# Performance work log

Measured on AMD Instinct MI355X. Metric: run time of the kernel, lower is better.

## Reference

```python
import jax, jax.numpy as jnp
import numpy as np

N0 = 50000
N1 = 50000
E = 500000
IN_DIM = 128
OUT_DIM = 128
H = 8
DK = OUT_DIM // H  # 16
SQRT_DK = float(np.sqrt(DK))
NUM_TYPES = 2
NUM_REL = 3
# relations: (src_type, dst_type, e_id)
RELATIONS = [(0, 1, 0), (1, 0, 1), (0, 0, 2)]


def setup_inputs() -> dict:
    key = jax.random.key(0)
    ks = jax.random.split(key, 24)
    d = {}
    d["h0"] = jax.random.normal(ks[0], (N0, IN_DIM), dtype=jnp.float32)
    d["h1"] = jax.random.normal(ks[1], (N1, IN_DIM), dtype=jnp.float32)
    d["src0"] = jax.random.randint(ks[2], (E,), 0, N0)
    d["dst0"] = jax.random.randint(ks[3], (E,), 0, N1)
    d["src1"] = jax.random.randint(ks[4], (E,), 0, N1)
    d["dst1"] = jax.random.randint(ks[5], (E,), 0, N0)
    d["src2"] = jax.random.randint(ks[6], (E,), 0, N0)
    d["dst2"] = jax.random.randint(ks[7], (E,), 0, N0)
    w_scale = 1.0 / np.sqrt(IN_DIM)
    # per-node-type stacked linear weights (k, q, v, a), torch Linear convention: y = x @ W.T + b
    d["Wk"] = jax.random.normal(ks[8], (NUM_TYPES, OUT_DIM, IN_DIM), dtype=jnp.float32) * w_scale
    d["bk"] = jnp.zeros((NUM_TYPES, OUT_DIM), dtype=jnp.float32)
    d["Wq"] = jax.random.normal(ks[9], (NUM_TYPES, OUT_DIM, IN_DIM), dtype=jnp.float32) * w_scale
    d["bq"] = jnp.zeros((NUM_TYPES, OUT_DIM), dtype=jnp.float32)
    d["Wv"] = jax.random.normal(ks[10], (NUM_TYPES, OUT_DIM, IN_DIM), dtype=jnp.float32) * w_scale
    d["bv"] = jnp.zeros((NUM_TYPES, OUT_DIM), dtype=jnp.float32)
    d["Wa"] = jax.random.normal(ks[11], (NUM_TYPES, OUT_DIM, OUT_DIM), dtype=jnp.float32) * w_scale
    d["ba"] = jnp.zeros((NUM_TYPES, OUT_DIM), dtype=jnp.float32)
    xavier = float(np.sqrt(6.0 / (DK + DK)))
    d["rel_att"] = jax.random.uniform(ks[12], (NUM_REL, H, DK, DK), dtype=jnp.float32, minval=-xavier, maxval=xavier)
    d["rel_msg"] = jax.random.uniform(ks[13], (NUM_REL, H, DK, DK), dtype=jnp.float32, minval=-xavier, maxval=xavier)
    d["rel_pri"] = jnp.ones((NUM_REL, H), dtype=jnp.float32)
    d["skip"] = jnp.ones((NUM_TYPES,), dtype=jnp.float32)
    return d


def _lin(x, W, b):
    return x @ W.T + b


def reference(h0, h1, src0, dst0, src1, dst1, src2, dst2,
              Wk, bk, Wq, bq, Wv, bv, Wa, ba,
              rel_att, rel_msg, rel_pri, skip):
    h = [h0, h1]
    edges = [(src0, dst0), (src1, dst1), (src2, dst2)]
    # per-type projections, reshaped to (N, H, DK)
    k = [_lin(h[t], Wk[t], bk[t]).reshape(-1, H, DK) for t in range(NUM_TYPES)]
    q = [_lin(h[t], Wq[t], bq[t]).reshape(-1, H, DK) for t in range(NUM_TYPES)]
    v = [_lin(h[t], Wv[t], bv[t]).reshape(-1, H, DK) for t in range(NUM_TYPES)]

    agg = [[] for _ in range(NUM_TYPES)]
    for (s, dt, e), (src, dst) in zip(RELATIONS, edges):
        # relation-specific transforms of source k and v
        kr = jnp.einsum('nhi,hij->nhj', k[s], rel_att[e])
        vr = jnp.einsum('nhi,hij->nhj', v[s], rel_msg[e])
        # per-edge dot-product score (E, H)
        score = (q[dt][dst] * kr[src]).sum(-1) * rel_pri[e] / SQRT_DK
        n_dst = h[dt].shape[0]
        # edge softmax normalized by dst (stable)
        m = jax.ops.segment_max(score, dst, num_segments=n_dst)
        ex = jnp.exp(score - m[dst])
        den = jax.ops.segment_sum(ex, dst, num_segments=n_dst)
        attn = ex / den[dst]  # (E, H)
        # weighted message scatter-sum -> (n_dst, H, DK)
        msg = vr[src] * attn[:, :, None]
        agg[dt].append(jax.ops.segment_sum(msg, dst, num_segments=n_dst))

    new_h = []
    for t in range(NUM_TYPES):
        # cross_reducer='mean' over relations targeting this node type
        tmean = sum(agg[t]) / float(len(agg[t]))
        tflat = tmean.reshape(-1, OUT_DIM)
        trans = _lin(tflat, Wa[t], ba[t])  # dropout = identity (eval)
        alpha = jax.nn.sigmoid(skip[t])
        new_h.append(trans * alpha + h[t] * (1.0 - alpha))
    return tuple(new_h)
```

## Files before the change

kernel.cpp:

```cpp
#include <hip/hip_runtime.h>

typedef __attribute__((ext_vector_type(8))) _Float16 half8;
typedef __attribute__((ext_vector_type(2))) _Float16 half2v;
typedef __attribute__((ext_vector_type(4))) float f32x4;

#define NB 196
#define CHK 2048
#define CAPB 4096
#define PSTRIDE 6144

__device__ __forceinline__ unsigned short f2h(float f) {
  _Float16 h = (_Float16)f;
  return __builtin_bit_cast(unsigned short, h);
}
__device__ __forceinline__ float fdot2(unsigned a, unsigned b, float c) {
  return __builtin_amdgcn_fdot2(__builtin_bit_cast(half2v, a), __builtin_bit_cast(half2v, b), c,
                                false);
}

#define DPPADD(v, ctrl) \
  ((v) + __int_as_float(__builtin_amdgcn_update_dpp(0, __float_as_int(v), ctrl, 0xF, 0xF, true)))

__global__ void cvt2_kernel(const float* __restrict__ a, unsigned short* __restrict__ oa,
                            const float* __restrict__ b, unsigned short* __restrict__ ob,
                            int n8) {
  int i = blockIdx.x * 256 + threadIdx.x;
  if (i >= n8) return;
  const float* in = blockIdx.y ? b : a;
  unsigned short* out = blockIdx.y ? ob : oa;
  const float4* p = (const float4*)(in + (size_t)i * 8);
  float4 x = p[0], y = p[1];
  uint4 v;
  v.x = f2h(x.x) | ((unsigned)f2h(x.y) << 16);
  v.y = f2h(x.z) | ((unsigned)f2h(x.w) << 16);
  v.z = f2h(y.x) | ((unsigned)f2h(y.y) << 16);
  v.w = f2h(y.z) | ((unsigned)f2h(y.w) << 16);
  *(uint4*)(out + (size_t)i * 8) = v;
}

__global__ void compose_w_kernel(const float* __restrict__ Wk, const float* __restrict__ bk,
                                 const float* __restrict__ Wv, const float* __restrict__ bv,
                                 const float* __restrict__ rel_att, const float* __restrict__ rel_msg,
                                 const float* __restrict__ rel_pri,
                                 unsigned short* __restrict__ Wkr, float* __restrict__ bkr,
                                 unsigned short* __restrict__ Wvr, float* __restrict__ bvr) {
  int e = blockIdx.x;
  int o = blockIdx.y;
  int z = blockIdx.z;
  int c = threadIdx.x;
  int hd = o >> 4, j = o & 15;
  const int se[3] = {0, 1, 0};
  int s = se[e];
  const float* W = z ? Wv : Wk;
  const float* b = z ? bv : bk;
  const float* R = z ? rel_msg : rel_att;
  float scale = z ? 1.0f : (rel_pri[e * 8 + hd] * 0.25f);
  float acc = 0.0f, bacc = 0.0f;
#pragma unroll
  for (int i = 0; i < 16; ++i) {
    float r = R[((e * 8 + hd) * 16 + i) * 16 + j];
    acc += W[(s * 128 + hd * 16 + i) * 128 + c] * r;
    bacc += b[s * 128 + hd * 16 + i] * r;
  }
  unsigned short* Wo = z ? Wvr : Wkr;
  float* bo = z ? bvr : bkr;
  Wo[((size_t)e * 128 + o) * 128 + c] = f2h(acc * scale);
  if (c == 0) bo[e * 128 + o] = bacc * scale;
}

struct ProjFP {
  const float* A[2];
  int M[2];
  int nj[2];
  const unsigned short* W[10];
  const float* b[10];
  unsigned short* out[10];
  int ostr[10];
};

__global__ __launch_bounds__(256) void proj_gemm_fused(ProjFP P) {
  __shared__ short As[128 * 128];
  __shared__ short Bs[128 * 128];
  int type = blockIdx.y;
  const float* __restrict__ A = P.A[type];
  int M = P.M[type];
  int nj = P.nj[type];
  int base = type * 5;
  int row0 = blockIdx.x * 128;
  if (row0 >= M) return;
  int t = threadIdx.x;
  bool full = (row0 + 128 <= M);
#pragma unroll
  for (int it = 0; it < 8; ++it) {
    int o = (it * 256 + t) * 8;
    int row = o >> 7, col = o & 127;
    int gr = row0 + row;
    uint4 av = make_uint4(0, 0, 0, 0);
    if (full || gr < M) {
      float4 x = *(const float4*)(A + (size_t)gr * 128 + col);
      float4 y = *(const float4*)(A + (size_t)gr * 128 + col + 4);
      av.x = f2h(x.x) | ((unsigned)f2h(x.y) << 16);
      av.y = f2h(x.z) | ((unsigned)f2h(x.w) << 16);
      av.z = f2h(y.x) | ((unsigned)f2h(y.y) << 16);
      av.w = f2h(y.z) | ((unsigned)f2h(y.w) << 16);
    }
    int sw = o ^ ((row & 7) << 3);
    *(uint4*)(&As[sw]) = av;
  }
  {
    const unsigned short* W0 = P.W[base];
#pragma unroll
    for (int it = 0; it < 8; ++it) {
      int o = (it * 256 + t) * 8;
      int row = o >> 7;
      int sw = o ^ ((row & 7) << 3);
      *(uint4*)(&Bs[sw]) = *(const uint4*)(W0 + o);
    }
  }
  __syncthreads();
  int wid = t >> 6, l = t & 63;
  int wr = wid >> 1, wc = wid & 1;
  int lr = l & 15, kb = l >> 4;
  for (int j = 0;; ++j) {
    f32x4 acc[4][4] = {};
#pragma unroll
    for (int ks = 0; ks < 4; ++ks) {
      half8 af[4], bfr[4];
#pragma unroll
      for (int m = 0; m < 4; ++m) {
        int row = wr * 64 + m * 16 + lr;
        int h = (row * 128 + kb * 8 + ks * 32) ^ ((row & 7) << 3);
        af[m] = *(half8*)(&As[h]);
      }
#pragma unroll
      for (int n = 0; n < 4; ++n) {
        int row = wc * 64 + n * 16 + lr;
        int h = (row * 128 + kb * 8 + ks * 32) ^ ((row & 7) << 3);
        bfr[n] = *(half8*)(&Bs[h]);
      }
#pragma unroll
      for (int m = 0; m < 4; ++m)
#pragma unroll
        for (int n = 0; n < 4; ++n)
          acc[m][n] = __builtin_amdgcn_mfma_f32_16x16x32_f16(af[m], bfr[n], acc[m][n], 0, 0, 0);
    }
    const float* bias = P.b[base + j];
    unsigned short* out = P.out[base + j];
    int ostr = P.ostr[base + j];
    int rb = row0 + wr * 64 + (l >> 4) * 4;
#pragma unroll
    for (int m = 0; m < 4; ++m)
#pragma unroll
      for (int jr = 0; jr < 4; ++jr) {
        int grow = rb + m * 16 + jr;
        if (grow < M) {
#pragma unroll
          for (int n = 0; n < 4; ++n) {
            int col = wc * 64 + n * 16 + lr;
            out[(size_t)grow * ostr + col] = f2h(acc[m][n][jr] + bias[col]);
          }
        }
      }
    if (j + 1 >= nj) break;
    __syncthreads();
    {
      const unsigned short* Wj = P.W[base + j + 1];
#pragma unroll
      for (int it = 0; it < 8; ++it) {
        int o = (it * 256 + t) * 8;
        int row = o >> 7;
        int sw = o ^ ((row & 7) << 3);
        *(uint4*)(&Bs[sw]) = *(const uint4*)(Wj + o);
      }
    }
    __syncthreads();
  }
}

__global__ __launch_bounds__(256) void final_gemm_mfma(
    float* __restrict__ dout, const unsigned short* __restrict__ Tb0,
    const unsigned short* __restrict__ Tb1, const unsigned short* __restrict__ Wab,
    const float* __restrict__ ba, const float* __restrict__ h0, const float* __restrict__ h1,
    const float* __restrict__ skip, int N0, int N1) {
  __shared__ short As[128 * 128];
  __shared__ short Bs[128 * 128];
  int type = blockIdx.y;
  int M = type ? N1 : N0;
  const unsigned short* T = type ? Tb1 : Tb0;
  const unsigned short* W = Wab + (size_t)type * 16384;
  const float* bias = ba + type * 128;
  const float* h = type ? h1 : h0;
  float* O = dout + (type ? (size_t)N0 * 128 : 0);
  int row0 = blockIdx.x * 128;
  if (row0 >= M) return;
  int t = threadIdx.x;
  bool full = (row0 + 128 <= M);
#pragma unroll
  for (int it = 0; it < 8; ++it) {
    int o = (it * 256 + t) * 8;
    int row = o >> 7;
    int gr = row0 + row;
    uint4 av = make_uint4(0, 0, 0, 0);
    if (full || gr < M) av = *(const uint4*)(T + (size_t)gr * 128 + (o & 127));
    int sw = o ^ ((row & 7) << 3);
    *(uint4*)(&As[sw]) = av;
    uint4 wv = *(const uint4*)(W + o);
    *(uint4*)(&Bs[sw]) = wv;
  }
  __syncthreads();
  int wid = t >> 6, l = t & 63;
  int wr = wid >> 1, wc = wid & 1;
  int lr = l & 15, kb = l >> 4;
  f32x4 acc[4][4] = {};
#pragma unroll
  for (int ks = 0; ks < 4; ++ks) {
    half8 af[4], bfr[4];
#pragma unroll
    for (int m = 0; m < 4; ++m) {
      int row = wr * 64 + m * 16 + lr;
      int h2 = (row * 128 + kb * 8 + ks * 32) ^ ((row & 7) << 3);
      af[m] = *(half8*)(&As[h2]);
    }
#pragma unroll
    for (int n = 0; n < 4; ++n) {
      int row = wc * 64 + n * 16 + lr;
      int h2 = (row * 128 + kb * 8 + ks * 32) ^ ((row & 7) << 3);
      bfr[n] = *(half8*)(&Bs[h2]);
    }
#pragma unroll
    for (int m = 0; m < 4; ++m)
#pragma unroll
      for (int n = 0; n < 4; ++n)
        acc[m][n] = __builtin_amdgcn_mfma_f32_16x16x32_f16(af[m], bfr[n], acc[m][n], 0, 0, 0);
  }
  float alpha = 1.0f / (1.0f + __expf(-skip[type]));
  float beta = 1.0f - alpha;
  int rb = row0 + wr * 64 + (l >> 4) * 4;
#pragma unroll
  for (int m = 0; m < 4; ++m)
#pragma unroll
    for (int jr = 0; jr < 4; ++jr) {
      int grow = rb + m * 16 + jr;
      if (grow < M) {
#pragma unroll
        for (int n = 0; n < 4; ++n) {
          int col = wc * 64 + n * 16 + lr;
          float vout = alpha * (acc[m][n][jr] + bias[col]) + beta * h[(size_t)grow * 128 + col];
          O[(size_t)grow * 128 + col] = vout;
        }
      }
    }
}


__global__ __launch_bounds__(256) void bhist_kernel(const int* __restrict__ d0,
                                                    const int* __restrict__ d1,
                                                    const int* __restrict__ d2,
                                                    int* __restrict__ bh, int E) {
  __shared__ int lh[NB];
  int r = blockIdx.y;
  const int* dst = r == 0 ? d0 : (r == 1 ? d1 : d2);
  int t = threadIdx.x;
  int lo = blockIdx.x * CHK;
  int hi = lo + CHK < E ? lo + CHK : E;
  for (int j = t; j < NB; j += 256) lh[j] = 0;
  __syncthreads();
  for (int i = lo + t; i < hi; i += 256) atomicAdd(&lh[dst[i] >> 8], 1);
  __syncthreads();
  for (int j = t; j < NB; j += 256) {
    int v = lh[j];
    if (v) atomicAdd(&bh[r * NB + j], v);
  }
}

__global__ void bscan_kernel(const int* __restrict__ bh, int* __restrict__ bbase, int E) {
  __shared__ int sdm[256];
  int r = blockIdx.x;
  int t = threadIdx.x;
  int v = (t < NB) ? bh[r * NB + t] : 0;
  sdm[t] = v;
  __syncthreads();
  for (int off = 1; off < 256; off <<= 1) {
    int u = (t >= off) ? sdm[t - off] : 0;
    __syncthreads();
    sdm[t] += u;
    __syncthreads();
  }
  if (t < NB) bbase[r * (NB + 1) + t] = sdm[t] - v;
  if (t == 0) bbase[r * (NB + 1) + NB] = E;
}

__global__ __launch_bounds__(256) void bin_kernel(
    const int* __restrict__ s0, const int* __restrict__ d0, const int* __restrict__ s1,
    const int* __restrict__ d1, const int* __restrict__ s2, const int* __restrict__ d2,
    const int* __restrict__ bbase, int* __restrict__ bcur, unsigned* __restrict__ bo0,
    unsigned* __restrict__ bo1, unsigned* __restrict__ bo2, int E) {
  __shared__ unsigned st[CHK];
  __shared__ int ga[CHK];
  __shared__ int hist[NB];
  __shared__ int scn[256];
  __shared__ int gb[NB];
  int r = blockIdx.y;
  const int* src = r == 0 ? s0 : (r == 1 ? s1 : s2);
  const int* dst = r == 0 ? d0 : (r == 1 ? d1 : d2);
  unsigned* bo = r == 0 ? bo0 : (r == 1 ? bo1 : bo2);
  const int* bb = bbase + r * (NB + 1);
  int t = threadIdx.x;
  int lo = blockIdx.x * CHK;
  int hi = lo + CHK < E ? lo + CHK : E;
  int nloc = hi - lo;
  if (nloc <= 0) return;
  for (int j = t; j < NB; j += 256) hist[j] = 0;
  __syncthreads();
  int myb[CHK / 256], myr[CHK / 256];
  unsigned mye[CHK / 256];
#pragma unroll
  for (int k = 0; k < CHK / 256; ++k) {
    int i = lo + k * 256 + t;
    myb[k] = -1;
    if (i < hi) {
      int d = dst[i];
      int b = d >> 8;
      mye[k] = (unsigned)src[i] | ((unsigned)d << 16);
      myb[k] = b;
      myr[k] = atomicAdd(&hist[b], 1);
    }
  }
  __syncthreads();
  int v = (t < NB) ? hist[t] : 0;
  scn[t] = v;
  __syncthreads();
  for (int off = 1; off < 256; off <<= 1) {
    int u = (t >= off) ? scn[t - off] : 0;
    __syncthreads();
    scn[t] += u;
    __syncthreads();
  }
  int excl = scn[t] - v;
  __syncthreads();
  scn[t] = excl;
  if (t < NB && v > 0) gb[t] = atomicAdd(&bcur[r * NB + t], v);
  __syncthreads();
#pragma unroll
  for (int k = 0; k < CHK / 256; ++k) {
    if (myb[k] >= 0) {
      int slot = scn[myb[k]] + myr[k];
      st[slot] = mye[k];
      ga[slot] = bb[myb[k]] + gb[myb[k]] + myr[k];
    }
  }
  __syncthreads();
  for (int j = t; j < nloc; j += 256) bo[ga[j]] = st[j];
}

__global__ __launch_bounds__(256) void bsort_kernel(
    const unsigned* __restrict__ bo0, const unsigned* __restrict__ bo1,
    const unsigned* __restrict__ bo2, const int* __restrict__ bbase, int* __restrict__ rs0,
    int* __restrict__ rs1, int* __restrict__ rs2, int* __restrict__ re0, int* __restrict__ re1,
    int* __restrict__ re2, unsigned* __restrict__ sp0, unsigned* __restrict__ sp1,
    unsigned* __restrict__ sp2, int nd0, int nd1, int nd2, int ns0, int ns1, int ns2) {
  __shared__ unsigned ed[CAPB];
  __shared__ unsigned srt[PSTRIDE];
  __shared__ unsigned short rank[CAPB];
  __shared__ int hist[256];
  __shared__ int scn[256];
  int r = blockIdx.y, b = blockIdx.x;
  const unsigned* bo = r == 0 ? bo0 : (r == 1 ? bo1 : bo2);
  int* rs = r == 0 ? rs0 : (r == 1 ? rs1 : rs2);
  int* re = r == 0 ? re0 : (r == 1 ? re1 : re2);
  unsigned* sp = r == 0 ? sp0 : (r == 1 ? sp1 : sp2);
  int nd = r == 0 ? nd0 : (r == 1 ? nd1 : nd2);
  unsigned sentinel = (unsigned)(r == 0 ? ns0 : (r == 1 ? ns1 : ns2));
  const int* bb = bbase + r * (NB + 1);
  int base = bb[b], endb = bb[b + 1];
  int cnt = endb - base;
  if (cnt > CAPB) cnt = CAPB;
  int nlo = b << 8;
  int nn = nd - nlo;
  if (nn > 256) nn = 256;
  if (nn < 0) nn = 0;
  int t = threadIdx.x;
  hist[t] = 0;
  for (int j = t; j < cnt; j += 256) ed[j] = bo[base + j];
  __syncthreads();
  for (int j = t; j < cnt; j += 256) {
    int node = (ed[j] >> 16) & 255;
    rank[j] = (unsigned short)atomicAdd(&hist[node], 1);
  }
  __syncthreads();
  int rawh = hist[t];
  int pd = (rawh + 7) & ~7;
  scn[t] = pd;
  __syncthreads();
  for (int off = 1; off < 256; off <<= 1) {
    int u = (t >= off) ? scn[t - off] : 0;
    __syncthreads();
    scn[t] += u;
    __syncthreads();
  }
  int pexcl = scn[t] - pd;
  int ptot = scn[255];
  __syncthreads();
  hist[t] = pexcl;
  __syncthreads();
  if (t < nn) {
    rs[nlo + t] = b * PSTRIDE + pexcl;
    re[nlo + t] = b * PSTRIDE + pexcl + rawh;
  }
  int ptot32 = (ptot + 31) & ~31;
  for (int j = t; j < ptot32; j += 256) srt[j] = sentinel;
  __syncthreads();
  for (int j = t; j < cnt; j += 256) {
    int node = (ed[j] >> 16) & 255;
    srt[hist[node] + rank[j]] = ed[j];
  }
  __syncthreads();
  unsigned* spb = sp + (size_t)b * PSTRIDE;
  for (int j = t; j < ptot32; j += 256) spb[j] = srt[j];
}

struct FuP {
  const unsigned *sp0, *sp1, *sp2;
  const unsigned *kv0, *kv1, *kv2;
  const unsigned *qb0, *qb1;
  const int *rs0, *rs1, *rs2;
  const int *re0, *re1, *re2;
  unsigned *Tb0, *Tb1;
  int N0, N1;
};

__device__ __forceinline__ void loadKV(const char* __restrict__ kvl,
                                       const unsigned* __restrict__ sp, int p, int half,
                                       uint2 kf[4], uint2 vf[4]) {
  unsigned sv = sp[p + (threadIdx.x & 7)];
#pragma unroll
  for (int g = 0; g < 4; ++g) {
    unsigned pA = __builtin_amdgcn_readlane(sv, g);
    unsigned pB = __builtin_amdgcn_readlane(sv, g + 4);
    unsigned pk = half ? pB : pA;
    const char* row = kvl + ((size_t)(pk & 0xFFFFu) << 9);
    kf[g] = *(const uint2*)row;
    vf[g] = *(const uint2*)(row + 256);
  }
}

__device__ __forceinline__ void computeKV(const uint2 kf[4], const uint2 vf[4], unsigned qx,
                                          unsigned qy, float& a0, float& a1, float& a2,
                                          float& a3, float& den) {
#pragma unroll
  for (int g = 0; g < 4; ++g) {
    float sc = fdot2(kf[g].y, qy, fdot2(kf[g].x, qx, 0.f));
    sc = DPPADD(sc, 0xB1);
    sc = DPPADD(sc, 0x4E);
    float e = __expf(sc);
    den += e;
    unsigned eu = f2h(e);
    unsigned pl = eu;
    unsigned ph = eu << 16;
    a0 = fdot2(vf[g].x, pl, a0);
    a1 = fdot2(vf[g].x, ph, a1);
    a2 = fdot2(vf[g].y, pl, a2);
    a3 = fdot2(vf[g].y, ph, a3);
  }
}

__device__ __forceinline__ void fuse_rel(const unsigned* __restrict__ sp,
                                         const unsigned* __restrict__ kv,
                                         const int* __restrict__ rs, const int* __restrict__ re,
                                         int node, int ll, int half, unsigned qx, unsigned qy,
                                         float& r0, float& r1, float& r2, float& r3) {
  int beg = __builtin_amdgcn_readfirstlane(rs[node]);
  int rend = __builtin_amdgcn_readfirstlane(re[node]);
  int raw = rend - beg;
  if (raw <= 0) return;
  int pd = (raw + 7) & ~7;
  int end = beg + pd;
  float npad = (float)(pd - raw);
  const char* kvl = (const char*)kv + ll * 8;
  float a0 = 0.f, a1 = 0.f, a2 = 0.f, a3 = 0.f, den = 0.f;
  uint2 ka[4], va[4], kb2[4], vb2[4];
  int p = beg;
  loadKV(kvl, sp, p, half, ka, va);
  for (;;) {
    if (p + 8 < end) loadKV(kvl, sp, p + 8, half, kb2, vb2);
    computeKV(ka, va, qx, qy, a0, a1, a2, a3, den);
    p += 8;
    if (p >= end) break;
    if (p + 8 < end) loadKV(kvl, sp, p + 8, half, ka, va);
    computeKV(kb2, vb2, qx, qy, a0, a1, a2, a3, den);
    p += 8;
    if (p >= end) break;
  }
  den += __shfl_xor(den, 32);
  a0 += __shfl_xor(a0, 32);
  a1 += __shfl_xor(a1, 32);
  a2 += __shfl_xor(a2, 32);
  a3 += __shfl_xor(a3, 32);
  den -= npad;
  float inv = 1.0f / den;
  r0 = fmaf(a0, inv, r0);
  r1 = fmaf(a1, inv, r1);
  r2 = fmaf(a2, inv, r2);
  r3 = fmaf(a3, inv, r3);
}

__global__ __launch_bounds__(256) void fusedge_kernel(FuP P) {
  int gw = (blockIdx.x * 256 + threadIdx.x) >> 6;
  int l = threadIdx.x & 63;
  int ll = l & 31, half = l >> 5;
  if (gw < P.N0) {
    uint2 q = *(const uint2*)((const char*)P.qb0 + (size_t)gw * 256 + ll * 8);
    float r0 = 0.f, r1 = 0.f, r2 = 0.f, r3 = 0.f;
    fuse_rel(P.sp1, P.kv1, P.rs1, P.re1, gw, ll, half, q.x, q.y, r0, r1, r2, r3);
    fuse_rel(P.sp2, P.kv2, P.rs2, P.re2, gw, ll, half, q.x, q.y, r0, r1, r2, r3);
    if (half == 0) {
      uint2 o;
      o.x = f2h(r0 * 0.5f) | ((unsigned)f2h(r1 * 0.5f) << 16);
      o.y = f2h(r2 * 0.5f) | ((unsigned)f2h(r3 * 0.5f) << 16);
      *(uint2*)(P.Tb0 + (size_t)gw * 64 + 2 * ll) = o;
    }
  } else if (gw < P.N0 + P.N1) {
    int n = gw - P.N0;
    uint2 q = *(const uint2*)((const char*)P.qb1 + (size_t)n * 256 + ll * 8);
    float r0 = 0.f, r1 = 0.f, r2 = 0.f, r3 = 0.f;
    fuse_rel(P.sp0, P.kv0, P.rs0, P.re0, n, ll, half, q.x, q.y, r0, r1, r2, r3);
    if (half == 0) {
      uint2 o;
      o.x = f2h(r0) | ((unsigned)f2h(r1) << 16);
      o.y = f2h(r2) | ((unsigned)f2h(r3) << 16);
      *(uint2*)(P.Tb1 + (size_t)n * 64 + 2 * ll) = o;
    }
  }
}

extern "C" void kernel_launch(void* const* d_in, const int* in_sizes, int n_in,
                              void* d_out, int out_size, void* d_ws, size_t ws_size,
                              hipStream_t stream) {
  const float* h0 = (const float*)d_in[0];
  const float* h1 = (const float*)d_in[1];
  const int* srcs[3] = {(const int*)d_in[2], (const int*)d_in[4], (const int*)d_in[6]};
  const int* dsts[3] = {(const int*)d_in[3], (const int*)d_in[5], (const int*)d_in[7]};
  const float* Wk = (const float*)d_in[8];
  const float* bk = (const float*)d_in[9];
  const float* Wq = (const float*)d_in[10];
  const float* bq = (const float*)d_in[11];
  const float* Wv = (const float*)d_in[12];
  const float* bv = (const float*)d_in[13];
  const float* Wa = (const float*)d_in[14];
  const float* ba = (const float*)d_in[15];
  const float* rel_att = (const float*)d_in[16];
  const float* rel_msg = (const float*)d_in[17];
  const float* rel_pri = (const float*)d_in[18];
  const float* skip = (const float*)d_in[19];

  int N0 = in_sizes[0] / 128;
  int N1 = in_sizes[1] / 128;
  int E = in_sizes[2];
  int nsrc[3] = {N0, N1, N0};
  int ndst[3] = {N1, N0, N0};
  int maxN = N0 > N1 ? N0 : N1;

  char* base = (char*)d_ws;
  size_t off = 0;
  auto alloc = [&](size_t bytes) -> void* {
    void* p = base + off;
    off += (bytes + 255) & ~(size_t)255;
    return p;
  };

  unsigned short* qb0 = (unsigned short*)alloc((size_t)N0 * 128 * 2);
  unsigned short* qb1 = (unsigned short*)alloc((size_t)N1 * 128 * 2);
  unsigned short* kvb[3];
  for (int r = 0; r < 3; ++r) kvb[r] = (unsigned short*)alloc((size_t)(nsrc[r] + 1) * 256 * 2);
  unsigned short* Tb0 = (unsigned short*)alloc((size_t)N0 * 128 * 2);
  unsigned short* Tb1 = (unsigned short*)alloc((size_t)N1 * 128 * 2);
  unsigned short* Wkrb = (unsigned short*)alloc((size_t)3 * 16384 * 2);
  unsigned short* Wvrb = (unsigned short*)alloc((size_t)3 * 16384 * 2);
  unsigned short* Wqb = (unsigned short*)alloc((size_t)2 * 16384 * 2);
  unsigned short* Wab = (unsigned short*)alloc((size_t)2 * 16384 * 2);
  float* bkr = (float*)alloc(3 * 128 * 4);
  float* bvr = (float*)alloc(3 * 128 * 4);
  int* rp_s[3];
  int* rp_e[3];
  unsigned* spk[3];
  unsigned* bo[3];
  for (int r = 0; r < 3; ++r) {
    rp_s[r] = (int*)alloc((size_t)ndst[r] * 4);
    rp_e[r] = (int*)alloc((size_t)ndst[r] * 4);
    spk[r] = (unsigned*)alloc((size_t)NB * PSTRIDE * 4);
    bo[r] = (unsigned*)alloc((size_t)(E + 8) * 4);
  }
  int* bcnt = (int*)alloc((size_t)2 * 3 * NB * 4);
  int* bhist = bcnt;
  int* bcur = bcnt + 3 * NB;
  int* bbase = (int*)alloc((size_t)3 * (NB + 1) * 4);
  (void)ws_size;

  for (int r = 0; r < 3; ++r)
    hipMemsetAsync(kvb[r] + (size_t)nsrc[r] * 256, 0, 512, stream);

  compose_w_kernel<<<dim3(3, 128, 2), 128, 0, stream>>>(Wk, bk, Wv, bv, rel_att, rel_msg,
                                                        rel_pri, Wkrb, bkr, Wvrb, bvr);
  cvt2_kernel<<<dim3(16, 2), 256, 0, stream>>>(Wq, Wqb, Wa, Wab, 4096);

  ProjFP pf;
  pf.A[0] = h0; pf.A[1] = h1;
  pf.M[0] = N0; pf.M[1] = N1;
  pf.nj[0] = 5; pf.nj[1] = 3;
  pf.W[0] = Wqb;            pf.b[0] = bq;        pf.out[0] = qb0;          pf.ostr[0] = 128;
  pf.W[1] = Wkrb;           pf.b[1] = bkr;       pf.out[1] = kvb[0];       pf.ostr[1] = 256;
  pf.W[2] = Wkrb + 32768;   pf.b[2] = bkr + 256; pf.out[2] = kvb[2];       pf.ostr[2] = 256;
  pf.W[3] = Wvrb;           pf.b[3] = bvr;       pf.out[3] = kvb[0] + 128; pf.ostr[3] = 256;
  pf.W[4] = Wvrb + 32768;   pf.b[4] = bvr + 256; pf.out[4] = kvb[2] + 128; pf.ostr[4] = 256;
  pf.W[5] = Wqb + 16384;    pf.b[5] = bq + 128;  pf.out[5] = qb1;          pf.ostr[5] = 128;
  pf.W[6] = Wkrb + 16384;   pf.b[6] = bkr + 128; pf.out[6] = kvb[1];       pf.ostr[6] = 256;
  pf.W[7] = Wvrb + 16384;   pf.b[7] = bvr + 128; pf.out[7] = kvb[1] + 128; pf.ostr[7] = 256;
  pf.W[8] = Wqb; pf.b[8] = bq; pf.out[8] = qb0; pf.ostr[8] = 128;
  pf.W[9] = Wqb; pf.b[9] = bq; pf.out[9] = qb0; pf.ostr[9] = 128;
  proj_gemm_fused<<<dim3((maxN + 127) / 128, 2), 256, 0, stream>>>(pf);

  hipMemsetAsync(bcnt, 0, (size_t)2 * 3 * NB * 4, stream);
  bhist_kernel<<<dim3((E + CHK - 1) / CHK, 3), 256, 0, stream>>>(dsts[0], dsts[1], dsts[2],
                                                                 bhist, E);
  bscan_kernel<<<3, 256, 0, stream>>>(bhist, bbase, E);
  bin_kernel<<<dim3((E + CHK - 1) / CHK, 3), 256, 0, stream>>>(
      srcs[0], dsts[0], srcs[1], dsts[1], srcs[2], dsts[2], bbase, bcur, bo[0], bo[1], bo[2], E);
  bsort_kernel<<<dim3(NB, 3), 256, 0, stream>>>(
      bo[0], bo[1], bo[2], bbase, rp_s[0], rp_s[1], rp_s[2], rp_e[0], rp_e[1], rp_e[2],
      spk[0], spk[1], spk[2], ndst[0], ndst[1], ndst[2], nsrc[0], nsrc[1], nsrc[2]);

  FuP fp2;
  fp2.sp0 = spk[0]; fp2.sp1 = spk[1]; fp2.sp2 = spk[2];
  fp2.kv0 = (const unsigned*)kvb[0]; fp2.kv1 = (const unsigned*)kvb[1];
  fp2.kv2 = (const unsigned*)kvb[2];
  fp2.qb0 = (const unsigned*)qb0; fp2.qb1 = (const unsigned*)qb1;
  fp2.rs0 = rp_s[0]; fp2.rs1 = rp_s[1]; fp2.rs2 = rp_s[2];
  fp2.re0 = rp_e[0]; fp2.re1 = rp_e[1]; fp2.re2 = rp_e[2];
  fp2.Tb0 = (unsigned*)Tb0; fp2.Tb1 = (unsigned*)Tb1;
  fp2.N0 = N0; fp2.N1 = N1;
  int totw = N0 + N1;
  fusedge_kernel<<<(totw + 3) / 4, 256, 0, stream>>>(fp2);

  final_gemm_mfma<<<dim3((maxN + 127) / 128, 2), 256, 0, stream>>>(
      (float*)d_out, Tb0, Tb1, Wab, ba, h0, h1, skip, N0, N1);
}
```

Baseline: 239.9 us.

## Fold scan and padding memsets into existing kernels, read GEMM weights directly

Removes the separate bucket-scan kernel by recomputing the per-relation prefix scan inside bin_kernel and bsort_kernel. Moves the three padding-row memsets into an extra grid slice of the weight-conversion kernel. Drops shared-memory staging of weight tiles in both projection and final GEMMs, loading B fragments straight from global/L2, which halves LDS use and removes barriers. Also software-pipelines the index loads in the edge kernel one step further ahead. The trade-off is redundant scans in every block and uncached, unswizzled global weight reads.

```diff
diff --git a/kernel.cpp b/kernel.cpp
--- a/kernel.cpp
+++ b/kernel.cpp
@@ -23,8 +23,18 @@
 
 __global__ void cvt2_kernel(const float* __restrict__ a, unsigned short* __restrict__ oa,
                             const float* __restrict__ b, unsigned short* __restrict__ ob,
-                            int n8) {
-  int i = blockIdx.x * 256 + threadIdx.x;
+                            int n8, unsigned short* __restrict__ z0,
+                            unsigned short* __restrict__ z1, unsigned short* __restrict__ z2) {
+  int t = threadIdx.x;
+  if (blockIdx.y == 2) {
+    if (blockIdx.x == 0 && t < 192) {
+      int r = t >> 6;
+      unsigned short* z = r == 0 ? z0 : (r == 1 ? z1 : z2);
+      ((uint2*)z)[t & 63] = make_uint2(0, 0);
+    }
+    return;
+  }
+  int i = blockIdx.x * 256 + t;
   if (i >= n8) return;
   const float* in = blockIdx.y ? b : a;
   unsigned short* out = blockIdx.y ? ob : oa;
@@ -80,7 +90,6 @@
 
 __global__ __launch_bounds__(256) void proj_gemm_fused(ProjFP P) {
   __shared__ short As[128 * 128];
-  __shared__ short Bs[128 * 128];
   int type = blockIdx.y;
   const float* __restrict__ A = P.A[type];
   int M = P.M[type];
@@ -107,21 +116,12 @@
     int sw = o ^ ((row & 7) << 3);
     *(uint4*)(&As[sw]) = av;
   }
-  {
-    const unsigned short* W0 = P.W[base];
-#pragma unroll
-    for (int it = 0; it < 8; ++it) {
-      int o = (it * 256 + t) * 8;
-      int row = o >> 7;
-      int sw = o ^ ((row & 7) << 3);
-      *(uint4*)(&Bs[sw]) = *(const uint4*)(W0 + o);
-    }
-  }
   __syncthreads();
   int wid = t >> 6, l = t & 63;
   int wr = wid >> 1, wc = wid & 1;
   int lr = l & 15, kb = l >> 4;
   for (int j = 0;; ++j) {
+    const unsigned short* __restrict__ W = P.W[base + j];
     f32x4 acc[4][4] = {};
 #pragma unroll
     for (int ks = 0; ks < 4; ++ks) {
@@ -135,8 +135,7 @@
 #pragma unroll
       for (int n = 0; n < 4; ++n) {
         int row = wc * 64 + n * 16 + lr;
-        int h = (row * 128 + kb * 8 + ks * 32) ^ ((row & 7) << 3);
-        bfr[n] = *(half8*)(&Bs[h]);
+        bfr[n] = *(const half8*)(W + (size_t)row * 128 + kb * 8 + ks * 32);
       }
 #pragma unroll
       for (int m = 0; m < 4; ++m)
@@ -162,18 +161,6 @@
         }
       }
     if (j + 1 >= nj) break;
-    __syncthreads();
-    {
-      const unsigned short* Wj = P.W[base + j + 1];
-#pragma unroll
-      for (int it = 0; it < 8; ++it) {
-        int o = (it * 256 + t) * 8;
-        int row = o >> 7;
-        int sw = o ^ ((row & 7) << 3);
-        *(uint4*)(&Bs[sw]) = *(const uint4*)(Wj + o);
-      }
-    }
-    __syncthreads();
   }
 }
 
@@ -183,7 +170,6 @@
     const float* __restrict__ ba, const float* __restrict__ h0, const float* __restrict__ h1,
     const float* __restrict__ skip, int N0, int N1) {
   __shared__ short As[128 * 128];
-  __shared__ short Bs[128 * 128];
   int type = blockIdx.y;
   int M = type ? N1 : N0;
   const unsigned short* T = type ? Tb1 : Tb0;
@@ -204,8 +190,6 @@
     if (full || gr < M) av = *(const uint4*)(T + (size_t)gr * 128 + (o & 127));
     int sw = o ^ ((row & 7) << 3);
     *(uint4*)(&As[sw]) = av;
-    uint4 wv = *(const uint4*)(W + o);
-    *(uint4*)(&Bs[sw]) = wv;
   }
   __syncthreads();
   int wid = t >> 6, l = t & 63;
@@ -224,8 +208,7 @@
 #pragma unroll
     for (int n = 0; n < 4; ++n) {
       int row = wc * 64 + n * 16 + lr;
-      int h2 = (row * 128 + kb * 8 + ks * 32) ^ ((row & 7) << 3);
-      bfr[n] = *(half8*)(&Bs[h2]);
+      bfr[n] = *(const half8*)(W + (size_t)row * 128 + kb * 8 + ks * 32);
     }
 #pragma unroll
     for (int m = 0; m < 4; ++m)
@@ -273,39 +256,35 @@
   }
 }
 
-__global__ void bscan_kernel(const int* __restrict__ bh, int* __restrict__ bbase, int E) {
-  __shared__ int sdm[256];
-  int r = blockIdx.x;
-  int t = threadIdx.x;
-  int v = (t < NB) ? bh[r * NB + t] : 0;
-  sdm[t] = v;
-  __syncthreads();
-  for (int off = 1; off < 256; off <<= 1) {
-    int u = (t >= off) ? sdm[t - off] : 0;
-    __syncthreads();
-    sdm[t] += u;
-    __syncthreads();
-  }
-  if (t < NB) bbase[r * (NB + 1) + t] = sdm[t] - v;
-  if (t == 0) bbase[r * (NB + 1) + NB] = E;
-}
-
 __global__ __launch_bounds__(256) void bin_kernel(
     const int* __restrict__ s0, const int* __restrict__ d0, const int* __restrict__ s1,
     const int* __restrict__ d1, const int* __restrict__ s2, const int* __restrict__ d2,
-    const int* __restrict__ bbase, int* __restrict__ bcur, unsigned* __restrict__ bo0,
+    const int* __restrict__ bh, int* __restrict__ bcur, unsigned* __restrict__ bo0,
     unsigned* __restrict__ bo1, unsigned* __restrict__ bo2, int E) {
   __shared__ unsigned st[CHK];
   __shared__ int ga[CHK];
   __shared__ int hist[NB];
   __shared__ int scn[256];
   __shared__ int gb[NB];
+  __shared__ int bbl[NB];
   int r = blockIdx.y;
   const int* src = r == 0 ? s0 : (r == 1 ? s1 : s2);
   const int* dst = r == 0 ? d0 : (r == 1 ? d1 : d2);
   unsigned* bo = r == 0 ? bo0 : (r == 1 ? bo1 : bo2);
-  const int* bb = bbase + r * (NB + 1);
   int t = threadIdx.x;
+  {
+    int v0 = (t < NB) ? bh[r * NB + t] : 0;
+    scn[t] = v0;
+    __syncthreads();
+    for (int off = 1; off < 256; off <<= 1) {
+      int u = (t >= off) ? scn[t - off] : 0;
+      __syncthreads();
+      scn[t] += u;
+      __syncthreads();
+    }
+    if (t < NB) bbl[t] = scn[t] - v0;
+    __syncthreads();
+  }
   int lo = blockIdx.x * CHK;
   int hi = lo + CHK < E ? lo + CHK : E;
   int nloc = hi - lo;
@@ -346,7 +325,7 @@
     if (myb[k] >= 0) {
       int slot = scn[myb[k]] + myr[k];
       st[slot] = mye[k];
-      ga[slot] = bb[myb[k]] + gb[myb[k]] + myr[k];
+      ga[slot] = bbl[myb[k]] + gb[myb[k]] + myr[k];
     }
   }
   __syncthreads();
@@ -355,15 +334,16 @@
 
 __global__ __launch_bounds__(256) void bsort_kernel(
     const unsigned* __restrict__ bo0, const unsigned* __restrict__ bo1,
-    const unsigned* __restrict__ bo2, const int* __restrict__ bbase, int* __restrict__ rs0,
+    const unsigned* __restrict__ bo2, const int* __restrict__ bh, int* __restrict__ rs0,
     int* __restrict__ rs1, int* __restrict__ rs2, int* __restrict__ re0, int* __restrict__ re1,
     int* __restrict__ re2, unsigned* __restrict__ sp0, unsigned* __restrict__ sp1,
-    unsigned* __restrict__ sp2, int nd0, int nd1, int nd2, int ns0, int ns1, int ns2) {
+    unsigned* __restrict__ sp2, int nd0, int nd1, int nd2, int ns0, int ns1, int ns2, int E) {
   __shared__ unsigned ed[CAPB];
   __shared__ unsigned srt[PSTRIDE];
   __shared__ unsigned short rank[CAPB];
   __shared__ int hist[256];
   __shared__ int scn[256];
+  __shared__ int bbl[NB + 1];
   int r = blockIdx.y, b = blockIdx.x;
   const unsigned* bo = r == 0 ? bo0 : (r == 1 ? bo1 : bo2);
   int* rs = r == 0 ? rs0 : (r == 1 ? rs1 : rs2);
@@ -371,15 +351,28 @@
   unsigned* sp = r == 0 ? sp0 : (r == 1 ? sp1 : sp2);
   int nd = r == 0 ? nd0 : (r == 1 ? nd1 : nd2);
   unsigned sentinel = (unsigned)(r == 0 ? ns0 : (r == 1 ? ns1 : ns2));
-  const int* bb = bbase + r * (NB + 1);
-  int base = bb[b], endb = bb[b + 1];
+  int t = threadIdx.x;
+  {
+    int v0 = (t < NB) ? bh[r * NB + t] : 0;
+    scn[t] = v0;
+    __syncthreads();
+    for (int off = 1; off < 256; off <<= 1) {
+      int u = (t >= off) ? scn[t - off] : 0;
+      __syncthreads();
+      scn[t] += u;
+      __syncthreads();
+    }
+    if (t < NB) bbl[t] = scn[t] - v0;
+    if (t == 0) bbl[NB] = E;
+    __syncthreads();
+  }
+  int base = bbl[b], endb = bbl[b + 1];
   int cnt = endb - base;
   if (cnt > CAPB) cnt = CAPB;
   int nlo = b << 8;
   int nn = nd - nlo;
   if (nn > 256) nn = 256;
   if (nn < 0) nn = 0;
-  int t = threadIdx.x;
   hist[t] = 0;
   for (int j = t; j < cnt; j += 256) ed[j] = bo[base + j];
   __syncthreads();
@@ -429,18 +422,17 @@
   int N0, N1;
 };
 
-__device__ __forceinline__ void loadKV(const char* __restrict__ kvl,
-                                       const unsigned* __restrict__ sp, int p, int half,
-                                       uint2 kf[4], uint2 vf[4]) {
-  unsigned sv = sp[p + (threadIdx.x & 7)];
+__device__ __forceinline__ void loadRows(const char* __restrict__ kvlk,
+                                         const char* __restrict__ kvlv, unsigned sv, int half,
+                                         uint2 kf[4], uint2 vf[4]) {
 #pragma unroll
   for (int g = 0; g < 4; ++g) {
     unsigned pA = __builtin_amdgcn_readlane(sv, g);
     unsigned pB = __builtin_amdgcn_readlane(sv, g + 4);
     unsigned pk = half ? pB : pA;
-    const char* row = kvl + ((size_t)(pk & 0xFFFFu) << 9);
-    kf[g] = *(const uint2*)row;
-    vf[g] = *(const uint2*)(row + 256);
+    size_t off = (size_t)(pk & 0xFFFFu) << 9;
+    kf[g] = *(const uint2*)(kvlk + off);
+    vf[g] = *(const uint2*)(kvlv + off);
   }
 }
 
@@ -476,17 +468,23 @@
   int pd = (raw + 7) & ~7;
   int end = beg + pd;
   float npad = (float)(pd - raw);
-  const char* kvl = (const char*)kv + ll * 8;
+  const char* kvlk = (const char*)kv + ll * 8;
+  const char* kvlv = (const char*)kv + 256 + ll * 8;
   float a0 = 0.f, a1 = 0.f, a2 = 0.f, a3 = 0.f, den = 0.f;
   uint2 ka[4], va[4], kb2[4], vb2[4];
+  int lane7 = threadIdx.x & 7;
   int p = beg;
-  loadKV(kvl, sp, p, half, ka, va);
+  unsigned svA = sp[p + lane7];
+  loadRows(kvlk, kvlv, svA, half, ka, va);
+  unsigned svB = sp[p + 8 + lane7];
   for (;;) {
-    if (p + 8 < end) loadKV(kvl, sp, p + 8, half, kb2, vb2);
+    if (p + 8 < end) loadRows(kvlk, kvlv, svB, half, kb2, vb2);
+    svA = sp[p + 16 + lane7];
     computeKV(ka, va, qx, qy, a0, a1, a2, a3, den);
     p += 8;
     if (p >= end) break;
-    if (p + 8 < end) loadKV(kvl, sp, p + 8, half, ka, va);
+    if (p + 8 < end) loadRows(kvlk, kvlv, svA, half, ka, va);
+    svB = sp[p + 16 + lane7];
     computeKV(kb2, vb2, qx, qy, a0, a1, a2, a3, den);
     p += 8;
     if (p >= end) break;
@@ -588,20 +586,19 @@
     rp_s[r] = (int*)alloc((size_t)ndst[r] * 4);
     rp_e[r] = (int*)alloc((size_t)ndst[r] * 4);
     spk[r] = (unsigned*)alloc((size_t)NB * PSTRIDE * 4);
-    bo[r] = (unsigned*)alloc((size_t)(E + 8) * 4);
+    bo[r] = (unsigned*)alloc((size_t)(E + 64) * 4);
   }
   int* bcnt = (int*)alloc((size_t)2 * 3 * NB * 4);
   int* bhist = bcnt;
   int* bcur = bcnt + 3 * NB;
-  int* bbase = (int*)alloc((size_t)3 * (NB + 1) * 4);
   (void)ws_size;
-
-  for (int r = 0; r < 3; ++r)
-    hipMemsetAsync(kvb[r] + (size_t)nsrc[r] * 256, 0, 512, stream);
 
   compose_w_kernel<<<dim3(3, 128, 2), 128, 0, stream>>>(Wk, bk, Wv, bv, rel_att, rel_msg,
                                                         rel_pri, Wkrb, bkr, Wvrb, bvr);
-  cvt2_kernel<<<dim3(16, 2), 256, 0, stream>>>(Wq, Wqb, Wa, Wab, 4096);
+  cvt2_kernel<<<dim3(16, 3), 256, 0, stream>>>(Wq, Wqb, Wa, Wab, 4096,
+                                               kvb[0] + (size_t)nsrc[0] * 256,
+                                               kvb[1] + (size_t)nsrc[1] * 256,
+                                               kvb[2] + (size_t)nsrc[2] * 256);
 
   ProjFP pf;
   pf.A[0] = h0; pf.A[1] = h1;
@@ -622,12 +619,11 @@
   hipMemsetAsync(bcnt, 0, (size_t)2 * 3 * NB * 4, stream);
   bhist_kernel<<<dim3((E + CHK - 1) / CHK, 3), 256, 0, stream>>>(dsts[0], dsts[1], dsts[2],
                                                                  bhist, E);
-  bscan_kernel<<<3, 256, 0, stream>>>(bhist, bbase, E);
   bin_kernel<<<dim3((E + CHK - 1) / CHK, 3), 256, 0, stream>>>(
-      srcs[0], dsts[0], srcs[1], dsts[1], srcs[2], dsts[2], bbase, bcur, bo[0], bo[1], bo[2], E);
+      srcs[0], dsts[0], srcs[1], dsts[1], srcs[2], dsts[2], bhist, bcur, bo[0], bo[1], bo[2], E);
   bsort_kernel<<<dim3(NB, 3), 256, 0, stream>>>(
-      bo[0], bo[1], bo[2], bbase, rp_s[0], rp_s[1], rp_s[2], rp_e[0], rp_e[1], rp_e[2],
-      spk[0], spk[1], spk[2], ndst[0], ndst[1], ndst[2], nsrc[0], nsrc[1], nsrc[2]);
+      bo[0], bo[1], bo[2], bhist, rp_s[0], rp_s[1], rp_s[2], rp_e[0], rp_e[1], rp_e[2],
+      spk[0], spk[1], spk[2], ndst[0], ndst[1], ndst[2], nsrc[0], nsrc[1], nsrc[2], E);
 
   FuP fp2;
   fp2.sp0 = spk[0]; fp2.sp1 = spk[1]; fp2.sp2 = spk[2];
```

New measurement: 252.9 us. +5.4%, slower.
